# Performance work log

Measured on AMD Instinct MI355X. Metric: run time of the kernel, lower is better.

Reference implementation:

```python
import jax, jax.numpy as jnp
import numpy as np

N_POS = 8192
BATCH = 4
N_GT = 512
EPS = 1e-6
P_EXP = -1.0  # generalized-mean exponent (p < 0)


def setup_inputs() -> dict:
    key = jax.random.key(0)
    k1, k2, k3 = jax.random.split(key, 3)
    dis_matrix = jax.random.uniform(k1, (N_POS, N_POS), dtype=jnp.float32)
    prob_map = jax.random.uniform(k2, (BATCH, N_POS), dtype=jnp.float32)
    gt = jax.random.randint(k3, (BATCH, N_GT), 0, N_POS, dtype=jnp.int64 if jax.config.jax_enable_x64 else jnp.int32)
    return {"prob_map": prob_map, "gt": gt, "dis_matrix": dis_matrix}


def reference(prob_map, gt, dis_matrix):
    max_dist = jnp.max(dis_matrix)
    # global min-max normalization with detached min/range (matches torch .detach())
    pmin = jax.lax.stop_gradient(jnp.min(prob_map))
    prange = jax.lax.stop_gradient(jnp.max(prob_map) - jnp.min(prob_map))
    prob = jnp.clip((prob_map - pmin) / prange, 0.0, 1.0)  # (B, N)

    # gather gt-indexed columns: dis_matrix[:, gt] -> (N, B, G) -> (B, N, G)
    D = jnp.transpose(jnp.take(dis_matrix, gt, axis=1), (1, 0, 2))

    n_est = prob.sum(axis=1)  # (B,)
    # term 1: (1/n_est) * sum_n p_n * min_g D[n, g]
    term1 = jnp.sum(prob * jnp.min(D, axis=2), axis=1) / (n_est + EPS)  # (B,)

    # term 2: generalized mean over pixel dim of weighted distance matrix
    w = (1.0 - prob)[:, :, None] * max_dist + prob[:, :, None] * D  # (B, N, G)
    minn = jnp.mean((w + EPS) ** P_EXP, axis=1) ** (1.0 / P_EXP)  # (B, G)
    term2 = jnp.mean(minn, axis=1)  # (B,)

    return jnp.mean(term1) + jnp.mean(term2)
```

## Files before the change

### kernel.cpp

```cpp
#include <hip/hip_runtime.h>
#include <math.h>

#define N_POS 8192
#define BATCH 4
#define N_GT 512
#define BG 2048
#define EPSV 1e-6f

#define KA_BLOCKS 1024
#define ROWS_A 8
#define KC_BLOCKS 1024
#define ROWS_C 8
#define RG 32
#define CHUNKS_PER_RG (KC_BLOCKS / RG)

#define WS_DPACK 0
#define WS_PARTS (N_POS * BG)
#define WS_PARTS2 (WS_PARTS + KC_BLOCKS * BG)
#define WS_MIND  (WS_PARTS2 + RG * BG)
#define WS_MAXP  (WS_MIND + BATCH * N_POS)
#define WS_SC    (WS_MAXP + KA_BLOCKS)

typedef __attribute__((ext_vector_type(4))) float f32x4;

__global__ __launch_bounds__(512, 8) void whd_kA(const float* __restrict__ dis,
                                                 const int* __restrict__ gt,
                                                 float* __restrict__ wsf) {
    __shared__ float rowbuf[N_POS];
    __shared__ unsigned short gtl[BG];
    __shared__ float smax[8];
    __shared__ float smin[8];
    const int t = threadIdx.x;
    const int wv = t >> 6, lane = t & 63;
    const int row0 = blockIdx.x * ROWS_A;
    float* dpack = wsf + WS_DPACK;
    float* minD = wsf + WS_MIND;

    for (int i = t; i < BG; i += 512) gtl[i] = (unsigned short)gt[i];

    f32x4 pre[4];
    {
        const f32x4* src = (const f32x4*)(dis + (size_t)row0 * N_POS);
        #pragma unroll
        for (int j = 0; j < 4; j++) pre[j] = __builtin_nontemporal_load(src + t + 512 * j);
    }
    __syncthreads();
    int c[4];
    #pragma unroll
    for (int k = 0; k < 4; k++) c[k] = gtl[4 * t + k];

    float tmax = -INFINITY;
    for (int r = 0; r < ROWS_A; r++) {
        const int n = row0 + r;
        f32x4* dstl = (f32x4*)rowbuf;
        #pragma unroll
        for (int j = 0; j < 4; j++) {
            f32x4 v = pre[j];
            tmax = fmaxf(tmax, fmaxf(fmaxf(v.x, v.y), fmaxf(v.z, v.w)));
            dstl[t + 512 * j] = v;
        }
        if (r + 1 < ROWS_A) {
            const f32x4* srcn = (const f32x4*)(dis + (size_t)(n + 1) * N_POS);
            #pragma unroll
            for (int j = 0; j < 4; j++) pre[j] = __builtin_nontemporal_load(srcn + t + 512 * j);
        }
        __syncthreads();
        float g0 = rowbuf[c[0]], g1 = rowbuf[c[1]], g2 = rowbuf[c[2]], g3 = rowbuf[c[3]];
        f32x4 pk; pk.x = g0; pk.y = g1; pk.z = g2; pk.w = g3;
        ((f32x4*)(dpack + (size_t)n * BG + 4 * t))[0] = pk;
        float m = fminf(fminf(g0, g1), fminf(g2, g3));
        #pragma unroll
        for (int off = 32; off; off >>= 1) m = fminf(m, __shfl_xor(m, off, 64));
        if (lane == 0) smin[wv] = m;
        __syncthreads();
        if (t < BATCH) minD[t * N_POS + n] = fminf(smin[2 * t], smin[2 * t + 1]);
    }
    #pragma unroll
    for (int off = 32; off; off >>= 1) tmax = fmaxf(tmax, __shfl_down(tmax, off, 64));
    if (lane == 0) smax[wv] = tmax;
    __syncthreads();
    if (t == 0) {
        float m = smax[0];
        #pragma unroll
        for (int i = 1; i < 8; i++) m = fmaxf(m, smax[i]);
        wsf[WS_MAXP + blockIdx.x] = m;
    }
}

__global__ __launch_bounds__(1024) void whd_kB(const float* __restrict__ prob,
                                               float* __restrict__ wsf) {
    __shared__ float sA[16], sB[16], sC[16];
    const int t = threadIdx.x, wv = t >> 6, lane = t & 63;

    float m = -INFINITY;
    for (int i = t; i < KA_BLOCKS; i += 1024) m = fmaxf(m, wsf[WS_MAXP + i]);
    #pragma unroll
    for (int off = 32; off; off >>= 1) m = fmaxf(m, __shfl_xor(m, off, 64));

    float lmin = INFINITY, lmax = -INFINITY;
    const f32x4* p4 = (const f32x4*)prob;
    for (int i = t; i < BATCH * N_POS / 4; i += 1024) {
        f32x4 v = p4[i];
        lmin = fminf(fminf(lmin, fminf(v.x, v.y)), fminf(v.z, v.w));
        lmax = fmaxf(fmaxf(lmax, fmaxf(v.x, v.y)), fmaxf(v.z, v.w));
    }
    #pragma unroll
    for (int off = 32; off; off >>= 1) {
        lmin = fminf(lmin, __shfl_xor(lmin, off, 64));
        lmax = fmaxf(lmax, __shfl_xor(lmax, off, 64));
    }
    if (lane == 0) { sA[wv] = m; sB[wv] = lmin; sC[wv] = lmax; }
    __syncthreads();
    if (t == 0) {
        float maxd = -INFINITY, mn = INFINITY, mx = -INFINITY;
        #pragma unroll
        for (int i = 0; i < 16; i++) {
            maxd = fmaxf(maxd, sA[i]); mn = fminf(mn, sB[i]); mx = fmaxf(mx, sC[i]);
        }
        wsf[WS_SC + 0] = maxd;
        wsf[WS_SC + 1] = mn;
        wsf[WS_SC + 2] = mx - mn;
        wsf[WS_SC + 11] = 0.f;
        wsf[WS_SC + 12] = 0.f;
        sB[0] = mn; sC[0] = 1.0f / (mx - mn);
    }
    __syncthreads();
    const float pmin = sB[0], invr = sC[0];

    const f32x4* d4 = (const f32x4*)(wsf + WS_MIND);
    for (int b = 0; b < BATCH; b++) {
        float sp = 0.f, spm = 0.f;
        for (int i = t; i < N_POS / 4; i += 1024) {
            f32x4 v = p4[b * (N_POS / 4) + i];
            f32x4 dm = d4[b * (N_POS / 4) + i];
            float p;
            p = fminf(fmaxf((v.x - pmin) * invr, 0.f), 1.f); sp += p; spm += p * dm.x;
            p = fminf(fmaxf((v.y - pmin) * invr, 0.f), 1.f); sp += p; spm += p * dm.y;
            p = fminf(fmaxf((v.z - pmin) * invr, 0.f), 1.f); sp += p; spm += p * dm.z;
            p = fminf(fmaxf((v.w - pmin) * invr, 0.f), 1.f); sp += p; spm += p * dm.w;
        }
        #pragma unroll
        for (int off = 32; off; off >>= 1) {
            sp += __shfl_xor(sp, off, 64);
            spm += __shfl_xor(spm, off, 64);
        }
        __syncthreads();
        if (lane == 0) { sA[wv] = sp; sB[wv] = spm; }
        __syncthreads();
        if (t == 0) {
            float a = 0.f, c2 = 0.f;
            #pragma unroll
            for (int i = 0; i < 16; i++) { a += sA[i]; c2 += sB[i]; }
            wsf[WS_SC + 3 + b] = a;
            wsf[WS_SC + 7 + b] = c2;
        }
    }
}

__global__ __launch_bounds__(256) void whd_kC(const float* __restrict__ prob,
                                              float* __restrict__ wsf) {
    const int t = threadIdx.x;
    const int wv = t >> 6;
    const int row0 = blockIdx.x * ROWS_C;
    const float* dpack = wsf + WS_DPACK;
    const float maxd = wsf[WS_SC + 0];
    const float pmin = wsf[WS_SC + 1];
    const float invr = 1.0f / wsf[WS_SC + 2];
    float acc[8];
    #pragma unroll
    for (int k = 0; k < 8; k++) acc[k] = 0.f;
    #pragma unroll
    for (int r = 0; r < ROWS_C; r++) {
        const int n = row0 + r;
        float p = (prob[wv * N_POS + n] - pmin) * invr;
        p = fminf(fmaxf(p, 0.f), 1.f);
        const f32x4* rp = (const f32x4*)(dpack + (size_t)n * BG + 8 * t);
        f32x4 v0 = __builtin_nontemporal_load(rp);
        f32x4 v1 = __builtin_nontemporal_load(rp + 1);
        acc[0] += 1.0f / (fmaf(p, v0.x - maxd, maxd) + EPSV);
        acc[1] += 1.0f / (fmaf(p, v0.y - maxd, maxd) + EPSV);
        acc[2] += 1.0f / (fmaf(p, v0.z - maxd, maxd) + EPSV);
        acc[3] += 1.0f / (fmaf(p, v0.w - maxd, maxd) + EPSV);
        acc[4] += 1.0f / (fmaf(p, v1.x - maxd, maxd) + EPSV);
        acc[5] += 1.0f / (fmaf(p, v1.y - maxd, maxd) + EPSV);
        acc[6] += 1.0f / (fmaf(p, v1.z - maxd, maxd) + EPSV);
        acc[7] += 1.0f / (fmaf(p, v1.w - maxd, maxd) + EPSV);
    }
    f32x4* op = (f32x4*)(wsf + WS_PARTS + (size_t)blockIdx.x * BG + 8 * t);
    f32x4 o0; o0.x = acc[0]; o0.y = acc[1]; o0.z = acc[2]; o0.w = acc[3];
    f32x4 o1; o1.x = acc[4]; o1.y = acc[5]; o1.z = acc[6]; o1.w = acc[7];
    op[0] = o0;
    op[1] = o1;
}

__global__ __launch_bounds__(256) void whd_kD1(float* __restrict__ wsf) {
    const int t = threadIdx.x;
    const int col = blockIdx.x * 256 + t;
    const int rg = blockIdx.y;
    const float* parts = wsf + WS_PARTS + (size_t)rg * CHUNKS_PER_RG * BG;
    float s = 0.f;
    #pragma unroll 8
    for (int ch = 0; ch < CHUNKS_PER_RG; ch++) s += parts[(size_t)ch * BG + col];
    wsf[WS_PARTS2 + (size_t)rg * BG + col] = s;
}

__global__ __launch_bounds__(256) void whd_kD2(float* __restrict__ wsf,
                                               float* __restrict__ out) {
    __shared__ float red[4];
    const int t = threadIdx.x;
    const int col = blockIdx.x * 256 + t;
    const float* p2 = wsf + WS_PARTS2;
    float s = 0.f;
    #pragma unroll
    for (int rg = 0; rg < RG; rg++) s += p2[(size_t)rg * BG + col];
    float val = (float)N_POS / s;
    #pragma unroll
    for (int off = 32; off; off >>= 1) val += __shfl_xor(val, off, 64);
    if ((t & 63) == 0) red[t >> 6] = val;
    __syncthreads();
    if (t == 0) {
        float blocksum = red[0] + red[1] + red[2] + red[3];
        atomicAdd(&wsf[WS_SC + 11], blocksum);
        __threadfence();
        unsigned prev = atomicAdd((unsigned*)(wsf + WS_SC + 12), 1u);
        if (prev == gridDim.x - 1) {
            float t2sum = atomicAdd(&wsf[WS_SC + 11], 0.0f);
            float term1 = 0.f;
            #pragma unroll
            for (int b = 0; b < BATCH; b++)
                term1 += wsf[WS_SC + 7 + b] / (wsf[WS_SC + 3 + b] + EPSV);
            out[0] = term1 * (1.0f / BATCH) + t2sum * (1.0f / BG);
        }
    }
}

extern "C" void kernel_launch(void* const* d_in, const int* in_sizes, int n_in,
                              void* d_out, int out_size, void* d_ws, size_t ws_size,
                              hipStream_t stream) {
    const float* prob = (const float*)d_in[0];
    const int* gt = (const int*)d_in[1];
    const float* dis = (const float*)d_in[2];
    float* out = (float*)d_out;
    float* wsf = (float*)d_ws;

    whd_kA<<<KA_BLOCKS, 512, 0, stream>>>(dis, gt, wsf);
    whd_kB<<<1, 1024, 0, stream>>>(prob, wsf);
    whd_kC<<<KC_BLOCKS, 256, 0, stream>>>(prob, wsf);
    whd_kD1<<<dim3(BG / 256, RG), 256, 0, stream>>>(wsf);
    whd_kD2<<<BG / 256, 256, 0, stream>>>(wsf, out);
}
```

Measured before the change: 397.4 us.

## Double-buffer row staging in LDS and drop per-row min barrier

Kernel A now stages rows in two alternating LDS buffers with two rows of register prefetch, so only one barrier per row is needed instead of two. The per-row min reduction across waves is removed: each wave writes its partial min to an expanded global minD array, and kernel B combines the two half-batch minima. gt indices are read straight from global as int4, which removes the LDS gt staging and its barrier. In exchange LDS use doubles to 64KB per block, which may lower occupancy, and register pressure rises from the extra prefetch.

```diff
diff --git a/kernel.cpp b/kernel.cpp
--- a/kernel.cpp
+++ b/kernel.cpp
@@ -18,62 +18,80 @@
 #define WS_PARTS (N_POS * BG)
 #define WS_PARTS2 (WS_PARTS + KC_BLOCKS * BG)
 #define WS_MIND  (WS_PARTS2 + RG * BG)
-#define WS_MAXP  (WS_MIND + BATCH * N_POS)
+#define WS_MAXP  (WS_MIND + 8 * N_POS)
 #define WS_SC    (WS_MAXP + KA_BLOCKS)
 
 typedef __attribute__((ext_vector_type(4))) float f32x4;
 
-__global__ __launch_bounds__(512, 8) void whd_kA(const float* __restrict__ dis,
-                                                 const int* __restrict__ gt,
-                                                 float* __restrict__ wsf) {
-    __shared__ float rowbuf[N_POS];
-    __shared__ unsigned short gtl[BG];
+__device__ __forceinline__ void rowbar() {
+    asm volatile("s_waitcnt lgkmcnt(0)" ::: "memory");
+    __builtin_amdgcn_s_barrier();
+    asm volatile("" ::: "memory");
+}
+
+__global__ __launch_bounds__(512) void whd_kA(const float* __restrict__ dis,
+                                              const int* __restrict__ gt,
+                                              float* __restrict__ wsf) {
+    __shared__ float rowbuf[2][N_POS];
     __shared__ float smax[8];
-    __shared__ float smin[8];
     const int t = threadIdx.x;
     const int wv = t >> 6, lane = t & 63;
     const int row0 = blockIdx.x * ROWS_A;
     float* dpack = wsf + WS_DPACK;
-    float* minD = wsf + WS_MIND;
-
-    for (int i = t; i < BG; i += 512) gtl[i] = (unsigned short)gt[i];
-
-    f32x4 pre[4];
+    float* minD2 = wsf + WS_MIND;
+
+    int c[4];
     {
-        const f32x4* src = (const f32x4*)(dis + (size_t)row0 * N_POS);
-        #pragma unroll
-        for (int j = 0; j < 4; j++) pre[j] = __builtin_nontemporal_load(src + t + 512 * j);
-    }
-    __syncthreads();
-    int c[4];
-    #pragma unroll
-    for (int k = 0; k < 4; k++) c[k] = gtl[4 * t + k];
+        const int4 ci = ((const int4*)gt)[t];
+        c[0] = ci.x; c[1] = ci.y; c[2] = ci.z; c[3] = ci.w;
+    }
+
+    f32x4 preA[4], preB[4];
+    {
+        const f32x4* s0 = (const f32x4*)(dis + (size_t)row0 * N_POS);
+        const f32x4* s1 = (const f32x4*)(dis + (size_t)(row0 + 1) * N_POS);
+        #pragma unroll
+        for (int j = 0; j < 4; j++) preA[j] = __builtin_nontemporal_load(s0 + t + 512 * j);
+        #pragma unroll
+        for (int j = 0; j < 4; j++) preB[j] = __builtin_nontemporal_load(s1 + t + 512 * j);
+    }
 
     float tmax = -INFINITY;
+    #pragma unroll
     for (int r = 0; r < ROWS_A; r++) {
         const int n = row0 + r;
-        f32x4* dstl = (f32x4*)rowbuf;
-        #pragma unroll
-        for (int j = 0; j < 4; j++) {
-            f32x4 v = pre[j];
-            tmax = fmaxf(tmax, fmaxf(fmaxf(v.x, v.y), fmaxf(v.z, v.w)));
-            dstl[t + 512 * j] = v;
-        }
-        if (r + 1 < ROWS_A) {
-            const f32x4* srcn = (const f32x4*)(dis + (size_t)(n + 1) * N_POS);
-            #pragma unroll
-            for (int j = 0; j < 4; j++) pre[j] = __builtin_nontemporal_load(srcn + t + 512 * j);
-        }
-        __syncthreads();
-        float g0 = rowbuf[c[0]], g1 = rowbuf[c[1]], g2 = rowbuf[c[2]], g3 = rowbuf[c[3]];
+        float* buf = rowbuf[r & 1];
+        if ((r & 1) == 0) {
+            #pragma unroll
+            for (int j = 0; j < 4; j++) ((f32x4*)buf)[t + 512 * j] = preA[j];
+            #pragma unroll
+            for (int j = 0; j < 4; j++)
+                tmax = fmaxf(tmax, fmaxf(fmaxf(preA[j].x, preA[j].y), fmaxf(preA[j].z, preA[j].w)));
+            if (r + 2 < ROWS_A) {
+                const f32x4* sn = (const f32x4*)(dis + (size_t)(n + 2) * N_POS);
+                #pragma unroll
+                for (int j = 0; j < 4; j++) preA[j] = __builtin_nontemporal_load(sn + t + 512 * j);
+            }
+        } else {
+            #pragma unroll
+            for (int j = 0; j < 4; j++) ((f32x4*)buf)[t + 512 * j] = preB[j];
+            #pragma unroll
+            for (int j = 0; j < 4; j++)
+                tmax = fmaxf(tmax, fmaxf(fmaxf(preB[j].x, preB[j].y), fmaxf(preB[j].z, preB[j].w)));
+            if (r + 2 < ROWS_A) {
+                const f32x4* sn = (const f32x4*)(dis + (size_t)(n + 2) * N_POS);
+                #pragma unroll
+                for (int j = 0; j < 4; j++) preB[j] = __builtin_nontemporal_load(sn + t + 512 * j);
+            }
+        }
+        rowbar();
+        float g0 = buf[c[0]], g1 = buf[c[1]], g2 = buf[c[2]], g3 = buf[c[3]];
         f32x4 pk; pk.x = g0; pk.y = g1; pk.z = g2; pk.w = g3;
         ((f32x4*)(dpack + (size_t)n * BG + 4 * t))[0] = pk;
         float m = fminf(fminf(g0, g1), fminf(g2, g3));
         #pragma unroll
         for (int off = 32; off; off >>= 1) m = fminf(m, __shfl_xor(m, off, 64));
-        if (lane == 0) smin[wv] = m;
-        __syncthreads();
-        if (t < BATCH) minD[t * N_POS + n] = fminf(smin[2 * t], smin[2 * t + 1]);
+        if (lane == 0) minD2[(size_t)wv * N_POS + n] = m;
     }
     #pragma unroll
     for (int off = 32; off; off >>= 1) tmax = fmaxf(tmax, __shfl_down(tmax, off, 64));
@@ -127,17 +145,18 @@
     __syncthreads();
     const float pmin = sB[0], invr = sC[0];
 
-    const f32x4* d4 = (const f32x4*)(wsf + WS_MIND);
     for (int b = 0; b < BATCH; b++) {
+        const f32x4* dA = (const f32x4*)(wsf + WS_MIND + (size_t)(2 * b) * N_POS);
+        const f32x4* dB = (const f32x4*)(wsf + WS_MIND + (size_t)(2 * b + 1) * N_POS);
         float sp = 0.f, spm = 0.f;
         for (int i = t; i < N_POS / 4; i += 1024) {
             f32x4 v = p4[b * (N_POS / 4) + i];
-            f32x4 dm = d4[b * (N_POS / 4) + i];
+            f32x4 da = dA[i], db = dB[i];
             float p;
-            p = fminf(fmaxf((v.x - pmin) * invr, 0.f), 1.f); sp += p; spm += p * dm.x;
-            p = fminf(fmaxf((v.y - pmin) * invr, 0.f), 1.f); sp += p; spm += p * dm.y;
-            p = fminf(fmaxf((v.z - pmin) * invr, 0.f), 1.f); sp += p; spm += p * dm.z;
-            p = fminf(fmaxf((v.w - pmin) * invr, 0.f), 1.f); sp += p; spm += p * dm.w;
+            p = fminf(fmaxf((v.x - pmin) * invr, 0.f), 1.f); sp += p; spm += p * fminf(da.x, db.x);
+            p = fminf(fmaxf((v.y - pmin) * invr, 0.f), 1.f); sp += p; spm += p * fminf(da.y, db.y);
+            p = fminf(fmaxf((v.z - pmin) * invr, 0.f), 1.f); sp += p; spm += p * fminf(da.z, db.z);
+            p = fminf(fmaxf((v.w - pmin) * invr, 0.f), 1.f); sp += p; spm += p * fminf(da.w, db.w);
         }
         #pragma unroll
         for (int off = 32; off; off >>= 1) {
```

After: 397.7 us. Within noise of the previous version (+0.1%).
